# Performance work log

Hardware: AMD Instinct MI355X
Metric: run time of the kernel (lower is better)

The kernel has to match this reference:

```python
import jax, jax.numpy as jnp
import numpy as np

L, E, H, D, F, B, CIN, N = 12, 128, 4, 32, 512, 64, 256, 257


def setup_inputs() -> dict:
    key = jax.random.key(0)
    ks = jax.random.split(key, 10)
    s = 0.02
    rn = lambda k, shape: jax.random.normal(k, shape, jnp.float32) * s
    return {
        "feat": jax.random.normal(ks[0], (B, CIN, 32, 32), jnp.float32),
        "conv_w": rn(ks[1], (E, CIN, 3, 3)),
        "conv_b": jnp.zeros((E,), jnp.float32),
        "pos_emb": rn(ks[2], (1, N, E)),
        "cls_token": rn(ks[3], (1, 1, E)),
        "ln1_s": jnp.ones((L, E), jnp.float32),
        "ln1_b": jnp.zeros((L, E), jnp.float32),
        "qkv_w": rn(ks[4], (L, 3 * E, E)),
        "qkv_b": jnp.zeros((L, 3 * E), jnp.float32),
        "proj_w": rn(ks[5], (L, E, E)),
        "proj_b": jnp.zeros((L, E), jnp.float32),
        "ln2_s": jnp.ones((L, E), jnp.float32),
        "ln2_b": jnp.zeros((L, E), jnp.float32),
        "ffn1_w": rn(ks[6], (L, F, E)),
        "ffn1_b": jnp.zeros((L, F), jnp.float32),
        "ffn2_w": rn(ks[7], (L, E, F)),
        "ffn2_b": jnp.zeros((L, E), jnp.float32),
        "fn_s": jnp.ones((E,), jnp.float32),
        "fn_b": jnp.zeros((E,), jnp.float32),
        "fc_w": rn(ks[8], (2, E)),
        "fc_b": jnp.zeros((2,), jnp.float32),
    }


def _ln(x, s, b, eps):
    m = jnp.mean(x, -1, keepdims=True)
    v = jnp.mean((x - m) ** 2, -1, keepdims=True)
    return (x - m) * jax.lax.rsqrt(v + eps) * s + b


def reference(feat, conv_w, conv_b, pos_emb, cls_token, ln1_s, ln1_b, qkv_w,
              qkv_b, proj_w, proj_b, ln2_s, ln2_b, ffn1_w, ffn1_b, ffn2_w,
              ffn2_b, fn_s, fn_b, fc_w, fc_b):
    # patch embed: 3x3 conv stride 2 -> 16x16 = 256 tokens
    emb = jax.lax.conv_general_dilated(
        feat, conv_w, (2, 2), ((1, 1), (1, 1)),
        dimension_numbers=("NCHW", "OIHW", "NCHW")) + conv_b[None, :, None, None]
    Bsz = emb.shape[0]
    emb = emb.reshape(Bsz, E, -1).transpose(0, 2, 1)  # [B, 256, E]
    x = jnp.concatenate([jnp.broadcast_to(cls_token, (Bsz, 1, E)), emb], axis=1)
    x = x + pos_emb  # [B, N, E]
    scale = (E // H) ** -0.5

    def block(x, p):
        l1s, l1b, qw, qb, pw, pb, l2s, l2b, w1, b1, w2, b2 = p
        h = _ln(x, l1s, l1b, 1e-5)
        qkv = (h @ qw.T + qb).reshape(Bsz, N, 3, H, D).transpose(2, 0, 3, 1, 4)
        q, k, v = qkv[0], qkv[1], qkv[2]  # [B, H, N, D]
        att = jax.nn.softmax(jnp.einsum("bhnd,bhmd->bhnm", q, k) * scale, axis=-1)
        o = jnp.einsum("bhnm,bhmd->bhnd", att, v).transpose(0, 2, 1, 3).reshape(Bsz, N, E)
        x = x + (o @ pw.T + pb)
        h2 = _ln(x, l2s, l2b, 1e-5)
        x = x + (jax.nn.gelu(h2 @ w1.T + b1, approximate=False) @ w2.T + b2)
        return x, None

    x, _ = jax.lax.scan(block, x, (ln1_s, ln1_b, qkv_w, qkv_b, proj_w, proj_b,
                                   ln2_s, ln2_b, ffn1_w, ffn1_b, ffn2_w, ffn2_b))
    x = _ln(x, fn_s, fn_b, 1e-6)
    out_feat = x[:, 0, :]
    out = out_feat @ fc_w.T + fc_b
    return (out, out_feat)
```

## Files before the change

### kernel.cpp

```cpp
#include <hip/hip_runtime.h>
#include <math.h>

constexpr int NP_ = 272;
constexpr int MP_ = 64 * NP_;
constexpr int TPB_ = 17;

typedef short short8 __attribute__((ext_vector_type(8)));
typedef float f32x4 __attribute__((ext_vector_type(4)));

__device__ inline short f2bs(float f) {
    unsigned u = __builtin_bit_cast(unsigned, f);
    unsigned r = (u + 0x7fffu + ((u >> 16) & 1u)) >> 16;
    return (short)r;
}

__device__ inline f32x4 mfma16(short8 a, short8 b, f32x4 c) {
    return __builtin_amdgcn_mfma_f32_16x16x32_bf16(a, b, c, 0, 0, 0);
}

__global__ void repack_w(const float* __restrict__ in, short* __restrict__ out, int Nn, int K, int total) {
    int o = blockIdx.x * 256 + threadIdx.x;
    if (o >= total) return;
    int per = Nn * K;
    int l = o / per, r = o % per;
    int chunk = r / (Nn * 8);
    int w = r % (Nn * 8);
    int n = w >> 3, j = w & 7;
    int k = chunk * 8 + j;
    out[o] = f2bs(in[(size_t)l * per + (size_t)n * K + k]);
}

__global__ void conv_w_perm(const float* __restrict__ w, short* __restrict__ wr) {
    int o = blockIdx.x * 256 + threadIdx.x;
    if (o >= 128 * 2304) return;
    int j = o & 7;
    int col = (o >> 3) & 127;
    int c = o >> 10;
    int qd = c & 3, cscb = c >> 2;
    int cs = cscb & 7, kykx = cscb >> 3;
    int cin = cs * 32 + qd * 8 + j;
    int ky = kykx / 3, kx = kykx % 3;
    wr[o] = f2bs(w[((col * 256 + cin) * 3 + ky) * 3 + kx]);
}

__global__ __launch_bounds__(256) void feat_nhwc(const float* __restrict__ feat, short* __restrict__ fp) {
    __shared__ float tile[32][33];
    int b = blockIdx.x >> 5, y = blockIdx.x & 31;
    int t = threadIdx.x;
    for (int c0 = 0; c0 < 256; c0 += 32) {
        int ci = t >> 5, x = t & 31;
        for (int cc = ci; cc < 32; cc += 8)
            tile[cc][x] = feat[((size_t)(b * 256 + c0 + cc) * 32 + y) * 32 + x];
        __syncthreads();
        for (int i = t; i < 1024; i += 256) {
            int c = i & 31, x2 = i >> 5;
            fp[((size_t)(b * 34 + y + 1) * 34 + x2 + 1) * 256 + c0 + c] = f2bs(tile[c][x2]);
        }
        __syncthreads();
    }
}

__global__ __launch_bounds__(256) void conv_gemm(const short* __restrict__ fp, const short* __restrict__ wr,
                                                 const float* __restrict__ cb, const float* __restrict__ pos,
                                                 float* __restrict__ X) {
    __shared__ __align__(16) short Ain[3 * 34 * 256];
    int b = blockIdx.x >> 4, oy = blockIdx.x & 15;
    int tid = threadIdx.x;
    for (int idx = tid; idx < 3 * 34 * 32; idx += 256) {
        int r = idx / 1088, rem = idx - r * 1088;
        int x = rem >> 5, c = rem & 31;
        short8 v = *(const short8*)(fp + ((size_t)(b * 34 + 2 * oy + r) * 34 + x) * 256 + c * 8);
        *(short8*)(Ain + (r * 34 + x) * 256 + ((c ^ ((x >> 1) & 7)) * 8)) = v;
    }
    __syncthreads();
    int wave = tid >> 6, lane = tid & 63;
    int ng = wave, lo = lane & 15, qd = lane >> 4;
    f32x4 acc[2] = {};
#pragma unroll
    for (int ky = 0; ky < 3; ++ky)
#pragma unroll
        for (int kx = 0; kx < 3; ++kx) {
            int sx = 2 * lo + kx;
            int arow = (ky * 34 + sx) * 256;
            int sw = (sx >> 1) & 7;
            const short* wb = wr + (((size_t)((ky * 3 + kx) * 8) * 4 + qd) * 128 + ng * 32 + lo) * 8;
#pragma unroll
            for (int cs = 0; cs < 8; ++cs) {
                short8 af = *(const short8*)(Ain + arow + (((cs * 4 + qd) ^ sw) * 8));
                short8 b0 = *(const short8*)(wb + (size_t)cs * 4096);
                short8 b1 = *(const short8*)(wb + (size_t)cs * 4096 + 128);
                acc[0] = mfma16(af, b0, acc[0]);
                acc[1] = mfma16(af, b1, acc[1]);
            }
        }
#pragma unroll
    for (int t = 0; t < 2; ++t) {
        int e = ng * 32 + t * 16 + lo;
        float bias = cb[e];
#pragma unroll
        for (int r = 0; r < 4; ++r) {
            int tok = 1 + oy * 16 + qd * 4 + r;
            X[((size_t)b * NP_ + tok) * 128 + e] = acc[t][r] + bias + pos[tok * 128 + e];
        }
    }
}

__global__ __launch_bounds__(256) void cls_init(const float* __restrict__ cls, const float* __restrict__ pos,
                                                float* __restrict__ X) {
    int b = blockIdx.x, tid = threadIdx.x;
    if (tid < 128) X[(size_t)b * NP_ * 128 + tid] = cls[tid] + pos[tid];
    for (int idx = tid; idx < 15 * 128; idx += 256)
        X[((size_t)b * NP_ + 257) * 128 + idx] = 0.f;
}

__device__ inline void ln_frags32(const float* Xl, const float* __restrict__ s, const float* __restrict__ bb,
                                  short* aF, int tid, float eps) {
    int wv = tid >> 6, lane = tid & 63;
    int r4 = lane & 3, c32 = lane >> 2;
    int row = wv * 4 + r4;
    const float* xr = Xl + row * 132 + c32 * 8;
    float4 a = *(const float4*)(xr);
    float4 b = *(const float4*)(xr + 4);
    float v[8] = {a.x, a.y, a.z, a.w, b.x, b.y, b.z, b.w};
    float sum = v[0] + v[1] + v[2] + v[3] + v[4] + v[5] + v[6] + v[7];
    sum += __shfl_xor(sum, 4); sum += __shfl_xor(sum, 8);
    sum += __shfl_xor(sum, 16); sum += __shfl_xor(sum, 32);
    float mean = sum * (1.f / 128.f);
    float vs = 0.f;
#pragma unroll
    for (int j = 0; j < 8; ++j) { float d = v[j] - mean; vs += d * d; }
    vs += __shfl_xor(vs, 4); vs += __shfl_xor(vs, 8);
    vs += __shfl_xor(vs, 16); vs += __shfl_xor(vs, 32);
    float rs = rsqrtf(vs * (1.f / 128.f) + eps);
    float4 s0 = *(const float4*)(s + c32 * 8), s1 = *(const float4*)(s + c32 * 8 + 4);
    float4 b0 = *(const float4*)(bb + c32 * 8), b1 = *(const float4*)(bb + c32 * 8 + 4);
    float sv[8] = {s0.x, s0.y, s0.z, s0.w, s1.x, s1.y, s1.z, s1.w};
    float bv[8] = {b0.x, b0.y, b0.z, b0.w, b1.x, b1.y, b1.z, b1.w};
    short8 o;
#pragma unroll
    for (int j = 0; j < 8; ++j) o[j] = f2bs((v[j] - mean) * rs * sv[j] + bv[j]);
    *(short8*)(aF + (((row >> 4) * 16 + c32) * 16 + (row & 15)) * 8) = o;
}

__device__ inline void qkv_stage(const short* aF, const short* __restrict__ wq, const float* __restrict__ qb,
                                 int mg, int wv, int lo, int qd,
                                 short* __restrict__ Qf, short* __restrict__ Kf, short* __restrict__ Vf) {
    int n0 = wv * 48;
    f32x4 acc[2][3] = {};
#pragma unroll
    for (int ki = 0; ki < 4; ++ki) {
        int kq = ki * 4 + qd;
        short8 bf[3];
#pragma unroll
        for (int t = 0; t < 3; ++t)
            bf[t] = *(const short8*)(wq + ((size_t)kq * 384 + n0 + t * 16 + lo) * 8);
#pragma unroll
        for (int mt = 0; mt < 2; ++mt) {
            short8 a = *(const short8*)(aF + ((mt * 16 + kq) * 16 + lo) * 8);
#pragma unroll
            for (int t = 0; t < 3; ++t) acc[mt][t] = mfma16(a, bf[t], acc[mt][t]);
        }
    }
#pragma unroll
    for (int mt = 0; mt < 2; ++mt)
#pragma unroll
        for (int t = 0; t < 3; ++t) {
            int n = n0 + t * 16 + lo;
            float bvv = qb[n];
            int seg = n >> 7, m = n & 127, h = m >> 5, d = m & 31;
            short* dst = (seg == 0) ? Qf : ((seg == 1) ? Kf : Vf);
#pragma unroll
            for (int r = 0; r < 4; ++r) {
                int row = mg * 32 + mt * 16 + qd * 4 + r;
                int bb2 = row / NP_, q = row - bb2 * NP_;
                dst[((size_t)(bb2 * 4 + h) * 4 + (d >> 3)) * (NP_ * 8) + q * 8 + (d & 7)] =
                    f2bs(acc[mt][t][r] + bvv);
            }
        }
}

__global__ __launch_bounds__(512, 4) void qkv0(const float* __restrict__ X, const short* __restrict__ wq,
                                               const float* __restrict__ qb, const float* __restrict__ ls,
                                               const float* __restrict__ lb,
                                               short* __restrict__ Qf, short* __restrict__ Kf,
                                               short* __restrict__ Vf) {
    __shared__ __align__(16) float Xl[32 * 132];
    __shared__ __align__(16) short aF[2 * 16 * 16 * 8];
    int mg = blockIdx.x, tid = threadIdx.x;
    for (int idx = tid; idx < 1024; idx += 512) {
        int tok = idx >> 5, c = idx & 31;
        *(float4*)(Xl + tok * 132 + c * 4) = *(const float4*)(X + (size_t)(mg * 32 + tok) * 128 + c * 4);
    }
    __syncthreads();
    ln_frags32(Xl, ls, lb, aF, tid, 1e-5f);
    __syncthreads();
    int wv = tid >> 6, lane = tid & 63;
    qkv_stage(aF, wq, qb, mg, wv, lane & 15, lane >> 4, Qf, Kf, Vf);
}

__global__ __launch_bounds__(256, 4) void tail_a(const short* __restrict__ Of, const short* __restrict__ wp,
                                                 const float* __restrict__ pb, const float* __restrict__ l2s,
                                                 const float* __restrict__ l2b, float* __restrict__ X,
                                                 short* __restrict__ Hf) {
    __shared__ __align__(16) short AL[2 * 2048];
    __shared__ __align__(16) float Xl[32 * 132];
    int mg = blockIdx.x, tid = threadIdx.x;
    const short* osrc = Of + (size_t)mg * 4096;
    for (int idx = tid; idx < 512; idx += 256)
        *(short8*)(AL + idx * 8) = *(const short8*)(osrc + idx * 8);
    for (int idx = tid; idx < 1024; idx += 256) {
        int tok = idx >> 5, c = idx & 31;
        *(float4*)(Xl + tok * 132 + c * 4) = *(const float4*)(X + (size_t)(mg * 32 + tok) * 128 + c * 4);
    }
    __syncthreads();
    int wv = tid >> 6, lane = tid & 63, lo = lane & 15, qd = lane >> 4;
    int n0 = wv * 32;
    f32x4 acc[2][2] = {};
#pragma unroll
    for (int ki = 0; ki < 4; ++ki) {
        int kq = ki * 4 + qd;
        short8 b0 = *(const short8*)(wp + ((size_t)kq * 128 + n0 + lo) * 8);
        short8 b1 = *(const short8*)(wp + ((size_t)kq * 128 + n0 + 16 + lo) * 8);
#pragma unroll
        for (int mt = 0; mt < 2; ++mt) {
            short8 a = *(const short8*)(AL + mt * 2048 + (kq * 16 + lo) * 8);
            acc[mt][0] = mfma16(a, b0, acc[mt][0]);
            acc[mt][1] = mfma16(a, b1, acc[mt][1]);
        }
    }
    float pb0 = pb[n0 + lo], pb1 = pb[n0 + 16 + lo];
#pragma unroll
    for (int mt = 0; mt < 2; ++mt)
#pragma unroll
        for (int r = 0; r < 4; ++r) {
            int row = mt * 16 + qd * 4 + r;
            Xl[row * 132 + n0 + lo] += acc[mt][0][r] + pb0;
            Xl[row * 132 + n0 + 16 + lo] += acc[mt][1][r] + pb1;
        }
    __syncthreads();
    for (int idx = tid; idx < 1024; idx += 256) {
        int tok = idx >> 5, c = idx & 31;
        *(float4*)(X + (size_t)(mg * 32 + tok) * 128 + c * 4) = *(const float4*)(Xl + tok * 132 + c * 4);
    }
    {
        int r8 = lane & 7, c16 = lane >> 3;
        int row = wv * 8 + r8;
        const float* xr = Xl + row * 132 + c16 * 16;
        float v[16]; float sum = 0.f;
#pragma unroll
        for (int p2 = 0; p2 < 4; ++p2) {
            float4 a = *(const float4*)(xr + p2 * 4);
            v[p2 * 4 + 0] = a.x; v[p2 * 4 + 1] = a.y; v[p2 * 4 + 2] = a.z; v[p2 * 4 + 3] = a.w;
            sum += a.x + a.y + a.z + a.w;
        }
        sum += __shfl_xor(sum, 8); sum += __shfl_xor(sum, 16); sum += __shfl_xor(sum, 32);
        float mean = sum * (1.f / 128.f);
        float vs = 0.f;
#pragma unroll
        for (int j = 0; j < 16; ++j) { float d = v[j] - mean; vs += d * d; }
        vs += __shfl_xor(vs, 8); vs += __shfl_xor(vs, 16); vs += __shfl_xor(vs, 32);
        float rs = rsqrtf(vs * (1.f / 128.f) + 1e-5f);
        float sv[16], bv[16];
#pragma unroll
        for (int p2 = 0; p2 < 4; ++p2) {
            float4 a = *(const float4*)(l2s + c16 * 16 + p2 * 4);
            float4 c = *(const float4*)(l2b + c16 * 16 + p2 * 4);
            sv[p2 * 4 + 0] = a.x; sv[p2 * 4 + 1] = a.y; sv[p2 * 4 + 2] = a.z; sv[p2 * 4 + 3] = a.w;
            bv[p2 * 4 + 0] = c.x; bv[p2 * 4 + 1] = c.y; bv[p2 * 4 + 2] = c.z; bv[p2 * 4 + 3] = c.w;
        }
        short8 o0, o1;
#pragma unroll
        for (int j = 0; j < 8; ++j) {
            o0[j] = f2bs((v[j] - mean) * rs * sv[j] + bv[j]);
            o1[j] = f2bs((v[j + 8] - mean) * rs * sv[j + 8] + bv[j + 8]);
        }
        int t2 = row >> 4, mr = row & 15;
        *(short8*)(Hf + (size_t)(2 * mg + t2) * 2048 + (c16 * 2) * 128 + mr * 8) = o0;
        *(short8*)(Hf + (size_t)(2 * mg + t2) * 2048 + (c16 * 2 + 1) * 128 + mr * 8) = o1;
    }
}

template <int LAST>
__global__ __launch_bounds__(512, 4) void tail_b(const short* __restrict__ Hf, const short* __restrict__ w1,
                                                 const float* __restrict__ b1, const short* __restrict__ w2,
                                                 const float* __restrict__ b2, float* __restrict__ X,
                                                 const float* __restrict__ l1s, const float* __restrict__ l1b,
                                                 const short* __restrict__ wq, const float* __restrict__ qb,
                                                 short* __restrict__ Qf, short* __restrict__ Kf,
                                                 short* __restrict__ Vf) {
    __shared__ __align__(16) short HfL[2 * 2048];
    __shared__ __align__(16) short U[128 * 136];
    __shared__ __align__(16) float Xl[32 * 132];
    __shared__ __align__(16) short aF[2 * 16 * 16 * 8];
    int mg = blockIdx.x, tid = threadIdx.x;
    const short* hsrc = Hf + (size_t)mg * 4096;
    for (int idx = tid; idx < 512; idx += 512)
        *(short8*)(HfL + idx * 8) = *(const short8*)(hsrc + idx * 8);
    for (int idx = tid; idx < 1024; idx += 512) {
        int tok = idx >> 5, c = idx & 31;
        *(float4*)(Xl + tok * 132 + c * 4) = *(const float4*)(X + (size_t)(mg * 32 + tok) * 128 + c * 4);
    }
    __syncthreads();
    int wv = tid >> 6, lane = tid & 63, lo = lane & 15, qd = lane >> 4;
    {
        int n0 = wv * 64;
        f32x4 fa[2][4] = {};
#pragma unroll
        for (int ki = 0; ki < 4; ++ki) {
            int kq = ki * 4 + qd;
            short8 bf[4];
#pragma unroll
            for (int t = 0; t < 4; ++t)
                bf[t] = *(const short8*)(w1 + ((size_t)kq * 512 + n0 + t * 16 + lo) * 8);
#pragma unroll
            for (int mt = 0; mt < 2; ++mt) {
                short8 a = *(const short8*)(HfL + mt * 2048 + (kq * 16 + lo) * 8);
#pragma unroll
                for (int t = 0; t < 4; ++t) fa[mt][t] = mfma16(a, bf[t], fa[mt][t]);
            }
        }
#pragma unroll
        for (int t = 0; t < 4; ++t) {
            int n = n0 + t * 16 + lo;
            float bvv = b1[n];
#pragma unroll
            for (int mt = 0; mt < 2; ++mt)
#pragma unroll
                for (int r = 0; r < 4; ++r) {
                    float x = fa[mt][t][r] + bvv;
                    float u = x * (0.7978845608f + 0.0356774081f * x * x);
                    x = x / (1.f + __expf(-2.f * u));
                    U[(mt * 64 + (n >> 3)) * 136 + (qd * 4 + r) * 8 + (n & 7)] = f2bs(x);
                }
        }
    }
    __syncthreads();
    {
        int n0 = wv * 16;
        f32x4 fa[2] = {};
#pragma unroll 4
        for (int ki = 0; ki < 16; ++ki) {
            int kq = ki * 4 + qd;
            short8 bf = *(const short8*)(w2 + ((size_t)kq * 128 + n0 + lo) * 8);
#pragma unroll
            for (int mt = 0; mt < 2; ++mt) {
                short8 a = *(const short8*)(U + (mt * 64 + kq) * 136 + lo * 8);
                fa[mt] = mfma16(a, bf, fa[mt]);
            }
        }
        float bvv = b2[n0 + lo];
#pragma unroll
        for (int mt = 0; mt < 2; ++mt)
#pragma unroll
            for (int r = 0; r < 4; ++r)
                Xl[(mt * 16 + qd * 4 + r) * 132 + n0 + lo] += fa[mt][r] + bvv;
    }
    __syncthreads();
    for (int idx = tid; idx < 1024; idx += 512) {
        int tok = idx >> 5, c = idx & 31;
        *(float4*)(X + (size_t)(mg * 32 + tok) * 128 + c * 4) = *(const float4*)(Xl + tok * 132 + c * 4);
    }
    if (LAST) return;
    ln_frags32(Xl, l1s, l1b, aF, tid, 1e-5f);
    __syncthreads();
    qkv_stage(aF, wq, qb, mg, wv, lo, qd, Qf, Kf, Vf);
}

__global__ __launch_bounds__(256) void attn(const short* __restrict__ Qf, const short* __restrict__ Kf,
                                            const short* __restrict__ Vf, short* __restrict__ Of) {
    __shared__ __align__(16) short Kl[4 * NP_ * 8];
    __shared__ __align__(16) short Vl[32 * 288];
    __shared__ __align__(16) short Pl[4 * 36 * 16 * 8];
    int b = blockIdx.x >> 3, h = (blockIdx.x >> 1) & 3, half = blockIdx.x & 1;
    int tid = threadIdx.x;
    const short* kf = Kf + (size_t)(b * 4 + h) * (4 * NP_ * 8);
    const short* vf = Vf + (size_t)(b * 4 + h) * (4 * NP_ * 8);
    const short* qf = Qf + (size_t)(b * 4 + h) * (4 * NP_ * 8);
    for (int idx = tid; idx < 1088; idx += 256)
        *(short8*)(Kl + idx * 8) = *(const short8*)(kf + idx * 8);
#pragma unroll
    for (int kq = 0; kq < 4; ++kq)
        for (int q = tid; q < NP_; q += 256) {
            short8 v = *(const short8*)(vf + ((size_t)kq * NP_ + q) * 8);
#pragma unroll
            for (int j = 0; j < 8; ++j) Vl[(kq * 8 + j) * 288 + q] = v[j];
        }
    for (int idx = tid; idx < 512; idx += 256) {
        int d = idx >> 4, c = idx & 15;
        Vl[d * 288 + 272 + c] = 0;
    }
    for (int idx = tid; idx < 128; idx += 256) {
        int w = idx >> 5, t = idx & 31;
        short8 z = {};
        *(short8*)(Pl + w * 4608 + 34 * 128 + t * 8) = z;
    }
    __syncthreads();
    int wv = tid >> 6, lane = tid & 63, lo = lane & 15, qd = lane >> 4;
    short* Pw = Pl + wv * 4608;
    const float scale = 0.17677669529663687f;
    for (int it = 0; it < 3; ++it) {
        int qt = it * 8 + half * 4 + wv;
        if (qt > 16) break;
        short8 qfr = *(const short8*)(qf + ((size_t)qd * NP_ + qt * 16 + lo) * 8);
        f32x4 sc[17];
#pragma unroll
        for (int kt = 0; kt < 17; ++kt) {
            short8 kfr = *(const short8*)(Kl + ((size_t)qd * NP_ + kt * 16 + lo) * 8);
            f32x4 z = {};
            sc[kt] = mfma16(qfr, kfr, z);
        }
        float mx[4] = {-1e30f, -1e30f, -1e30f, -1e30f};
#pragma unroll
        for (int kt = 0; kt < 17; ++kt) {
            bool valid = (kt * 16 + lo) < 257;
#pragma unroll
            for (int r = 0; r < 4; ++r) {
                float v2 = valid ? sc[kt][r] * scale : -1e30f;
                sc[kt][r] = v2;
                mx[r] = fmaxf(mx[r], v2);
            }
        }
#pragma unroll
        for (int r = 0; r < 4; ++r) {
            mx[r] = fmaxf(mx[r], __shfl_xor(mx[r], 1));
            mx[r] = fmaxf(mx[r], __shfl_xor(mx[r], 2));
            mx[r] = fmaxf(mx[r], __shfl_xor(mx[r], 4));
            mx[r] = fmaxf(mx[r], __shfl_xor(mx[r], 8));
        }
        float l[4] = {0.f, 0.f, 0.f, 0.f};
#pragma unroll
        for (int kt = 0; kt < 17; ++kt)
#pragma unroll
            for (int r = 0; r < 4; ++r) {
                float p = __expf(sc[kt][r] - mx[r]);
                sc[kt][r] = p;
                l[r] += p;
            }
#pragma unroll
        for (int r = 0; r < 4; ++r) {
            l[r] += __shfl_xor(l[r], 1);
            l[r] += __shfl_xor(l[r], 2);
            l[r] += __shfl_xor(l[r], 4);
            l[r] += __shfl_xor(l[r], 8);
        }
        float rl[4];
#pragma unroll
        for (int r = 0; r < 4; ++r) rl[r] = 1.f / l[r];
#pragma unroll
        for (int kt = 0; kt < 17; ++kt)
#pragma unroll
            for (int r = 0; r < 4; ++r) {
                int key = kt * 16 + lo;
                Pw[((key >> 3) * 16 + qd * 4 + r) * 8 + (key & 7)] = f2bs(sc[kt][r] * rl[r]);
            }
        f32x4 oa[2] = {};
#pragma unroll
        for (int ks = 0; ks < 9; ++ks) {
            short8 pf = *(const short8*)(Pw + ((ks * 4 + qd) * 16 + lo) * 8);
#pragma unroll
            for (int nt = 0; nt < 2; ++nt) {
                short8 vfr = *(const short8*)(Vl + (nt * 16 + lo) * 288 + ks * 32 + qd * 8);
                oa[nt] = mfma16(pf, vfr, oa[nt]);
            }
        }
        int tile = b * TPB_ + qt;
#pragma unroll
        for (int nt = 0; nt < 2; ++nt)
#pragma unroll
            for (int r = 0; r < 4; ++r) {
                int qq = qt * 16 + qd * 4 + r;
                if (qq <= 256) {
                    int col = h * 32 + nt * 16 + lo;
                    Of[(size_t)tile * 2048 + (col >> 3) * 128 + (qd * 4 + r) * 8 + (col & 7)] = f2bs(oa[nt][r]);
                }
            }
    }
}

__global__ __launch_bounds__(64) void final_head(const float* __restrict__ X, const float* __restrict__ fs,
                                                 const float* __restrict__ fb, const float* __restrict__ fcw,
                                                 const float* __restrict__ fcb, float* __restrict__ out) {
    int b = blockIdx.x, lane = threadIdx.x;
    float2 v = *(const float2*)(X + (size_t)b * NP_ * 128 + lane * 2);
    float sum = v.x + v.y;
#pragma unroll
    for (int m = 1; m < 64; m <<= 1) sum += __shfl_xor(sum, m);
    float mean = sum * (1.f / 128.f);
    float d0 = v.x - mean, d1 = v.y - mean;
    float vs = d0 * d0 + d1 * d1;
#pragma unroll
    for (int m = 1; m < 64; m <<= 1) vs += __shfl_xor(vs, m);
    float rs = rsqrtf(vs * (1.f / 128.f) + 1e-6f);
    int e = lane * 2;
    float f0 = d0 * rs * fs[e] + fb[e];
    float f1 = d1 * rs * fs[e + 1] + fb[e + 1];
    out[128 + b * 128 + e] = f0;
    out[128 + b * 128 + e + 1] = f1;
    float p0 = f0 * fcw[e] + f1 * fcw[e + 1];
    float p1 = f0 * fcw[128 + e] + f1 * fcw[128 + e + 1];
#pragma unroll
    for (int m = 1; m < 64; m <<= 1) {
        p0 += __shfl_xor(p0, m);
        p1 += __shfl_xor(p1, m);
    }
    if (lane == 0) {
        out[b * 2 + 0] = p0 + fcb[0];
        out[b * 2 + 1] = p1 + fcb[1];
    }
}

extern "C" void kernel_launch(void* const* d_in, const int* in_sizes, int n_in,
                              void* d_out, int out_size, void* d_ws, size_t ws_size,
                              hipStream_t stream) {
    const float* feat    = (const float*)d_in[0];
    const float* conv_w  = (const float*)d_in[1];
    const float* conv_b  = (const float*)d_in[2];
    const float* pos_emb = (const float*)d_in[3];
    const float* cls_tok = (const float*)d_in[4];
    const float* ln1_s   = (const float*)d_in[5];
    const float* ln1_b   = (const float*)d_in[6];
    const float* qkv_w   = (const float*)d_in[7];
    const float* qkv_b   = (const float*)d_in[8];
    const float* proj_w  = (const float*)d_in[9];
    const float* proj_b  = (const float*)d_in[10];
    const float* ln2_s   = (const float*)d_in[11];
    const float* ln2_b   = (const float*)d_in[12];
    const float* ffn1_w  = (const float*)d_in[13];
    const float* ffn1_b  = (const float*)d_in[14];
    const float* ffn2_w  = (const float*)d_in[15];
    const float* ffn2_b  = (const float*)d_in[16];
    const float* fn_s    = (const float*)d_in[17];
    const float* fn_b    = (const float*)d_in[18];
    const float* fc_w    = (const float*)d_in[19];
    const float* fc_b    = (const float*)d_in[20];

    char* p = (char*)d_ws;
    auto alloc = [&](size_t bytes) { char* r = p; p += (bytes + 255) & ~(size_t)255; return r; };
    short* wq  = (short*)alloc((size_t)589824 * 2);
    short* wp  = (short*)alloc((size_t)196608 * 2);
    short* w1  = (short*)alloc((size_t)786432 * 2);
    short* w2  = (short*)alloc((size_t)786432 * 2);
    short* wc  = (short*)alloc((size_t)294912 * 2);
    short* fpd = (short*)alloc((size_t)64 * 34 * 34 * 256 * 2);
    float* X   = (float*)alloc((size_t)MP_ * 128 * 4);
    short* Qf  = (short*)alloc((size_t)64 * 16 * NP_ * 8 * 2);
    short* Kf  = (short*)alloc((size_t)64 * 16 * NP_ * 8 * 2);
    short* Vf  = (short*)alloc((size_t)64 * 16 * NP_ * 8 * 2);
    short* Of  = (short*)alloc((size_t)(MP_ / 16) * 2048 * 2);
    short* Hf  = (short*)alloc((size_t)(MP_ / 16) * 2048 * 2);

    hipMemsetAsync(fpd, 0, (size_t)64 * 34 * 34 * 256 * 2, stream);
    repack_w<<<2304, 256, 0, stream>>>(qkv_w, wq, 384, 128, 589824);
    repack_w<<<768, 256, 0, stream>>>(proj_w, wp, 128, 128, 196608);
    repack_w<<<3072, 256, 0, stream>>>(ffn1_w, w1, 512, 128, 786432);
    repack_w<<<3072, 256, 0, stream>>>(ffn2_w, w2, 128, 512, 786432);
    conv_w_perm<<<1152, 256, 0, stream>>>(conv_w, wc);
    feat_nhwc<<<64 * 32, 256, 0, stream>>>(feat, fpd);
    conv_gemm<<<1024, 256, 0, stream>>>(fpd, wc, conv_b, pos_emb, X);
    cls_init<<<64, 256, 0, stream>>>(cls_tok, pos_emb, X);

    qkv0<<<544, 512, 0, stream>>>(X, wq, qkv_b, ln1_s, ln1_b, Qf, Kf, Vf);
    for (int l = 0; l < 12; ++l) {
        attn<<<512, 256, 0, stream>>>(Qf, Kf, Vf, Of);
        tail_a<<<544, 256, 0, stream>>>(Of, wp + (size_t)l * 16384, proj_b + l * 128,
                                        ln2_s + l * 128, ln2_b + l * 128, X, Hf);
        if (l < 11)
            tail_b<0><<<544, 512, 0, stream>>>(Hf, w1 + (size_t)l * 65536, ffn1_b + l * 512,
                                               w2 + (size_t)l * 65536, ffn2_b + l * 128, X,
                                               ln1_s + (l + 1) * 128, ln1_b + (l + 1) * 128,
                                               wq + (size_t)(l + 1) * 49152, qkv_b + (l + 1) * 384,
                                               Qf, Kf, Vf);
        else
            tail_b<1><<<544, 512, 0, stream>>>(Hf, w1 + (size_t)l * 65536, ffn1_b + l * 512,
                                               w2 + (size_t)l * 65536, ffn2_b + l * 128, X,
                                               ln1_s, ln1_b, wq, qkv_b, Qf, Kf, Vf);
    }
    final_head<<<64, 64, 0, stream>>>(X, fn_s, fn_b, fc_w, fc_b, (float*)d_out);
}
```

Measured before the change: 870.4 us.

## Fuse proj/LN2/FFN/QKV into one 16-row layer kernel, transpose V layout

Measured after the change: 864.2 us. Within noise of the previous version (-0.7%).

```diff
diff --git a/kernel.cpp b/kernel.cpp
--- a/kernel.cpp
+++ b/kernel.cpp
@@ -18,29 +18,55 @@
     return __builtin_amdgcn_mfma_f32_16x16x32_bf16(a, b, c, 0, 0, 0);
 }
 
-__global__ void repack_w(const float* __restrict__ in, short* __restrict__ out, int Nn, int K, int total) {
+__global__ void repack_all(const float* __restrict__ qkvw, const float* __restrict__ projw,
+                           const float* __restrict__ f1w, const float* __restrict__ f2w,
+                           const float* __restrict__ convw,
+                           short* __restrict__ wq, short* __restrict__ wp,
+                           short* __restrict__ w1, short* __restrict__ w2,
+                           short* __restrict__ wc) {
     int o = blockIdx.x * 256 + threadIdx.x;
-    if (o >= total) return;
-    int per = Nn * K;
-    int l = o / per, r = o % per;
-    int chunk = r / (Nn * 8);
-    int w = r % (Nn * 8);
-    int n = w >> 3, j = w & 7;
-    int k = chunk * 8 + j;
-    out[o] = f2bs(in[(size_t)l * per + (size_t)n * K + k]);
-}
-
-__global__ void conv_w_perm(const float* __restrict__ w, short* __restrict__ wr) {
-    int o = blockIdx.x * 256 + threadIdx.x;
-    if (o >= 128 * 2304) return;
-    int j = o & 7;
-    int col = (o >> 3) & 127;
-    int c = o >> 10;
-    int qd = c & 3, cscb = c >> 2;
-    int cs = cscb & 7, kykx = cscb >> 3;
-    int cin = cs * 32 + qd * 8 + j;
-    int ky = kykx / 3, kx = kykx % 3;
-    wr[o] = f2bs(w[((col * 256 + cin) * 3 + ky) * 3 + kx]);
+    if (o < 589824) {
+        int l = o / 49152, r = o % 49152;
+        int chunk = r / 3072, w = r % 3072;
+        int n = w >> 3, k = chunk * 8 + (w & 7);
+        wq[o] = f2bs(qkvw[(size_t)l * 49152 + n * 128 + k]);
+        return;
+    }
+    o -= 589824;
+    if (o < 196608) {
+        int l = o / 16384, r = o % 16384;
+        int chunk = r / 1024, w = r % 1024;
+        int n = w >> 3, k = chunk * 8 + (w & 7);
+        wp[o] = f2bs(projw[(size_t)l * 16384 + n * 128 + k]);
+        return;
+    }
+    o -= 196608;
+    if (o < 786432) {
+        int l = o / 65536, r = o % 65536;
+        int chunk = r / 4096, w = r % 4096;
+        int n = w >> 3, k = chunk * 8 + (w & 7);
+        w1[o] = f2bs(f1w[(size_t)l * 65536 + n * 128 + k]);
+        return;
+    }
+    o -= 786432;
+    if (o < 786432) {
+        int l = o / 65536, r = o % 65536;
+        int chunk = r / 1024, w = r % 1024;
+        int n = w >> 3, k = chunk * 8 + (w & 7);
+        w2[o] = f2bs(f2w[(size_t)l * 65536 + n * 512 + k]);
+        return;
+    }
+    o -= 786432;
+    if (o < 294912) {
+        int j = o & 7;
+        int col = (o >> 3) & 127;
+        int c = o >> 10;
+        int qd = c & 3, cscb = c >> 2;
+        int cs = cscb & 7, kykx = cscb >> 3;
+        int cin = cs * 32 + qd * 8 + j;
+        int ky = kykx / 3, kx = kykx % 3;
+        wc[o] = f2bs(convw[((col * 256 + cin) * 3 + ky) * 3 + kx]);
+    }
 }
 
 __global__ __launch_bounds__(256) void feat_nhwc(const float* __restrict__ feat, short* __restrict__ fp) {
@@ -58,6 +84,16 @@
         }
         __syncthreads();
     }
+    short* rowp = fp + (size_t)(b * 34 + y + 1) * 34 * 256;
+    for (int c = t; c < 256; c += 256) { rowp[c] = 0; rowp[33 * 256 + c] = 0; }
+    if (y == 0) {
+        short* r0 = fp + (size_t)(b * 34) * 34 * 256;
+        for (int i = t; i < 34 * 256; i += 256) r0[i] = 0;
+    }
+    if (y == 31) {
+        short* r33 = fp + (size_t)(b * 34 + 33) * 34 * 256;
+        for (int i = t; i < 34 * 256; i += 256) r33[i] = 0;
+    }
 }
 
 __global__ __launch_bounds__(256) void conv_gemm(const short* __restrict__ fp, const short* __restrict__ wr,
@@ -113,8 +149,8 @@
         X[((size_t)b * NP_ + 257) * 128 + idx] = 0.f;
 }
 
-__device__ inline void ln_frags32(const float* Xl, const float* __restrict__ s, const float* __restrict__ bb,
-                                  short* aF, int tid, float eps) {
+__device__ inline void ln_tile16(const float* Xl, const float* __restrict__ s, const float* __restrict__ bb,
+                                 short* SB, int tid, float eps) {
     int wv = tid >> 6, lane = tid & 63;
     int r4 = lane & 3, c32 = lane >> 2;
     int row = wv * 4 + r4;
@@ -139,264 +175,188 @@
     short8 o;
 #pragma unroll
     for (int j = 0; j < 8; ++j) o[j] = f2bs((v[j] - mean) * rs * sv[j] + bv[j]);
-    *(short8*)(aF + (((row >> 4) * 16 + c32) * 16 + (row & 15)) * 8) = o;
-}
-
-__device__ inline void qkv_stage(const short* aF, const short* __restrict__ wq, const float* __restrict__ qb,
-                                 int mg, int wv, int lo, int qd,
-                                 short* __restrict__ Qf, short* __restrict__ Kf, short* __restrict__ Vf) {
-    int n0 = wv * 48;
-    f32x4 acc[2][3] = {};
+    *(short8*)(SB + (c32 * 16 + row) * 8) = o;
+}
+
+__device__ inline void qkv_stage16(const short* SB, const short* __restrict__ wq, const float* __restrict__ qb,
+                                   int mg, int wv, int lo, int qd,
+                                   short* __restrict__ Qf, short* __restrict__ Kf, short* __restrict__ Vt) {
+    int n0 = wv * 96;
+    f32x4 acc[6] = {};
 #pragma unroll
     for (int ki = 0; ki < 4; ++ki) {
         int kq = ki * 4 + qd;
-        short8 bf[3];
-#pragma unroll
-        for (int t = 0; t < 3; ++t)
-            bf[t] = *(const short8*)(wq + ((size_t)kq * 384 + n0 + t * 16 + lo) * 8);
-#pragma unroll
-        for (int mt = 0; mt < 2; ++mt) {
-            short8 a = *(const short8*)(aF + ((mt * 16 + kq) * 16 + lo) * 8);
-#pragma unroll
-            for (int t = 0; t < 3; ++t) acc[mt][t] = mfma16(a, bf[t], acc[mt][t]);
-        }
-    }
-#pragma unroll
-    for (int mt = 0; mt < 2; ++mt)
-#pragma unroll
-        for (int t = 0; t < 3; ++t) {
-            int n = n0 + t * 16 + lo;
-            float bvv = qb[n];
-            int seg = n >> 7, m = n & 127, h = m >> 5, d = m & 31;
-            short* dst = (seg == 0) ? Qf : ((seg == 1) ? Kf : Vf);
-#pragma unroll
-            for (int r = 0; r < 4; ++r) {
-                int row = mg * 32 + mt * 16 + qd * 4 + r;
-                int bb2 = row / NP_, q = row - bb2 * NP_;
-                dst[((size_t)(bb2 * 4 + h) * 4 + (d >> 3)) * (NP_ * 8) + q * 8 + (d & 7)] =
-                    f2bs(acc[mt][t][r] + bvv);
-            }
-        }
-}
-
-__global__ __launch_bounds__(512, 4) void qkv0(const float* __restrict__ X, const short* __restrict__ wq,
+        short8 a = *(const short8*)(SB + (kq * 16 + lo) * 8);
+#pragma unroll
+        for (int t = 0; t < 6; ++t) {
+            short8 bf = *(const short8*)(wq + ((size_t)kq * 384 + n0 + t * 16 + lo) * 8);
+            acc[t] = mfma16(a, bf, acc[t]);
+        }
+    }
+#pragma unroll
+    for (int t = 0; t < 6; ++t) {
+        int n = n0 + t * 16 + lo;
+        float bvv = qb[n];
+        int seg = n >> 7, m = n & 127, h = m >> 5, d = m & 31;
+#pragma unroll
+        for (int r = 0; r < 4; ++r) {
+            int row = mg * 16 + qd * 4 + r;
+            int bb2 = row / NP_, q = row - bb2 * NP_;
+            short val = f2bs(acc[t][r] + bvv);
+            if (seg == 2)
+                Vt[((size_t)(bb2 * 4 + h) * 32 + d) * NP_ + q] = val;
+            else
+                (seg ? Kf : Qf)[((size_t)(bb2 * 4 + h) * 4 + (d >> 3)) * (NP_ * 8) + q * 8 + (d & 7)] = val;
+        }
+    }
+}
+
+__global__ __launch_bounds__(256, 4) void qkv0(const float* __restrict__ X, const short* __restrict__ wq,
                                                const float* __restrict__ qb, const float* __restrict__ ls,
                                                const float* __restrict__ lb,
                                                short* __restrict__ Qf, short* __restrict__ Kf,
-                                               short* __restrict__ Vf) {
-    __shared__ __align__(16) float Xl[32 * 132];
-    __shared__ __align__(16) short aF[2 * 16 * 16 * 8];
+                                               short* __restrict__ Vt) {
+    __shared__ __align__(16) float Xl[16 * 132];
+    __shared__ __align__(16) short SB[2048];
     int mg = blockIdx.x, tid = threadIdx.x;
-    for (int idx = tid; idx < 1024; idx += 512) {
+    for (int idx = tid; idx < 512; idx += 256) {
         int tok = idx >> 5, c = idx & 31;
-        *(float4*)(Xl + tok * 132 + c * 4) = *(const float4*)(X + (size_t)(mg * 32 + tok) * 128 + c * 4);
-    }
-    __syncthreads();
-    ln_frags32(Xl, ls, lb, aF, tid, 1e-5f);
+        *(float4*)(Xl + tok * 132 + c * 4) = *(const float4*)(X + (size_t)(mg * 16 + tok) * 128 + c * 4);
+    }
+    __syncthreads();
+    ln_tile16(Xl, ls, lb, SB, tid, 1e-5f);
     __syncthreads();
     int wv = tid >> 6, lane = tid & 63;
-    qkv_stage(aF, wq, qb, mg, wv, lane & 15, lane >> 4, Qf, Kf, Vf);
-}
-
-__global__ __launch_bounds__(256, 4) void tail_a(const short* __restrict__ Of, const short* __restrict__ wp,
-                                                 const float* __restrict__ pb, const float* __restrict__ l2s,
-                                                 const float* __restrict__ l2b, float* __restrict__ X,
-                                                 short* __restrict__ Hf) {
-    __shared__ __align__(16) short AL[2 * 2048];
-    __shared__ __align__(16) float Xl[32 * 132];
+    qkv_stage16(SB, wq, qb, mg, wv, lane & 15, lane >> 4, Qf, Kf, Vt);
+}
+
+template <int LAST>
+__global__ __launch_bounds__(256, 4) void layer_tail(
+    const short* __restrict__ Of, const short* __restrict__ wp, const float* __restrict__ pb,
+    const float* __restrict__ l2s, const float* __restrict__ l2b,
+    const short* __restrict__ w1, const float* __restrict__ b1,
+    const short* __restrict__ w2, const float* __restrict__ b2,
+    float* __restrict__ X,
+    const float* __restrict__ l1s, const float* __restrict__ l1b,
+    const short* __restrict__ wq, const float* __restrict__ qb,
+    short* __restrict__ Qf, short* __restrict__ Kf, short* __restrict__ Vt) {
+    __shared__ __align__(16) short SB[2048];
+    __shared__ __align__(16) float Xl[16 * 132];
+    __shared__ __align__(16) short Uh[32 * 136];
     int mg = blockIdx.x, tid = threadIdx.x;
-    const short* osrc = Of + (size_t)mg * 4096;
-    for (int idx = tid; idx < 512; idx += 256)
-        *(short8*)(AL + idx * 8) = *(const short8*)(osrc + idx * 8);
-    for (int idx = tid; idx < 1024; idx += 256) {
+    const short* osrc = Of + (size_t)mg * 2048;
+    for (int idx = tid; idx < 256; idx += 256)
+        *(short8*)(SB + idx * 8) = *(const short8*)(osrc + idx * 8);
+    for (int idx = tid; idx < 512; idx += 256) {
         int tok = idx >> 5, c = idx & 31;
-        *(float4*)(Xl + tok * 132 + c * 4) = *(const float4*)(X + (size_t)(mg * 32 + tok) * 128 + c * 4);
-    }
-    __syncthreads();
-    int wv = tid >> 6, lane = tid & 63, lo = lane & 15, qd = lane >> 4;
-    int n0 = wv * 32;
-    f32x4 acc[2][2] = {};
-#pragma unroll
-    for (int ki = 0; ki < 4; ++ki) {
-        int kq = ki * 4 + qd;
-        short8 b0 = *(const short8*)(wp + ((size_t)kq * 128 + n0 + lo) * 8);
-        short8 b1 = *(const short8*)(wp + ((size_t)kq * 128 + n0 + 16 + lo) * 8);
-#pragma unroll
-        for (int mt = 0; mt < 2; ++mt) {
-            short8 a = *(const short8*)(AL + mt * 2048 + (kq * 16 + lo) * 8);
-            acc[mt][0] = mfma16(a, b0, acc[mt][0]);
-            acc[mt][1] = mfma16(a, b1, acc[mt][1]);
-        }
-    }
-    float pb0 = pb[n0 + lo], pb1 = pb[n0 + 16 + lo];
-#pragma unroll
-    for (int mt = 0; mt < 2; ++mt)
-#pragma unroll
-        for (int r = 0; r < 4; ++r) {
-            int row = mt * 16 + qd * 4 + r;
-            Xl[row * 132 + n0 + lo] += acc[mt][0][r] + pb0;
-            Xl[row * 132 + n0 + 16 + lo] += acc[mt][1][r] + pb1;
-        }
-    __syncthreads();
-    for (int idx = tid; idx < 1024; idx += 256) {
-        int tok = idx >> 5, c = idx & 31;
-        *(float4*)(X + (size_t)(mg * 32 + tok) * 128 + c * 4) = *(const float4*)(Xl + tok * 132 + c * 4);
-    }
-    {
-        int r8 = lane & 7, c16 = lane >> 3;
-        int row = wv * 8 + r8;
-        const float* xr = Xl + row * 132 + c16 * 16;
-        float v[16]; float sum = 0.f;
-#pragma unroll
-        for (int p2 = 0; p2 < 4; ++p2) {
-            float4 a = *(const float4*)(xr + p2 * 4);
-            v[p2 * 4 + 0] = a.x; v[p2 * 4 + 1] = a.y; v[p2 * 4 + 2] = a.z; v[p2 * 4 + 3] = a.w;
-            sum += a.x + a.y + a.z + a.w;
-        }
-        sum += __shfl_xor(sum, 8); sum += __shfl_xor(sum, 16); sum += __shfl_xor(sum, 32);
-        float mean = sum * (1.f / 128.f);
-        float vs = 0.f;
-#pragma unroll
-        for (int j = 0; j < 16; ++j) { float d = v[j] - mean; vs += d * d; }
-        vs += __shfl_xor(vs, 8); vs += __shfl_xor(vs, 16); vs += __shfl_xor(vs, 32);
-        float rs = rsqrtf(vs * (1.f / 128.f) + 1e-5f);
-        float sv[16], bv[16];
-#pragma unroll
-        for (int p2 = 0; p2 < 4; ++p2) {
-            float4 a = *(const float4*)(l2s + c16 * 16 + p2 * 4);
-            float4 c = *(const float4*)(l2b + c16 * 16 + p2 * 4);
-            sv[p2 * 4 + 0] = a.x; sv[p2 * 4 + 1] = a.y; sv[p2 * 4 + 2] = a.z; sv[p2 * 4 + 3] = a.w;
-            bv[p2 * 4 + 0] = c.x; bv[p2 * 4 + 1] = c.y; bv[p2 * 4 + 2] = c.z; bv[p2 * 4 + 3] = c.w;
-        }
-        short8 o0, o1;
-#pragma unroll
-        for (int j = 0; j < 8; ++j) {
-            o0[j] = f2bs((v[j] - mean) * rs * sv[j] + bv[j]);
-            o1[j] = f2bs((v[j + 8] - mean) * rs * sv[j + 8] + bv[j + 8]);
-        }
-        int t2 = row >> 4, mr = row & 15;
-        *(short8*)(Hf + (size_t)(2 * mg + t2) * 2048 + (c16 * 2) * 128 + mr * 8) = o0;
-        *(short8*)(Hf + (size_t)(2 * mg + t2) * 2048 + (c16 * 2 + 1) * 128 + mr * 8) = o1;
-    }
-}
-
-template <int LAST>
-__global__ __launch_bounds__(512, 4) void tail_b(const short* __restrict__ Hf, const short* __restrict__ w1,
-                                                 const float* __restrict__ b1, const short* __restrict__ w2,
-                                                 const float* __restrict__ b2, float* __restrict__ X,
-                                                 const float* __restrict__ l1s, const float* __restrict__ l1b,
-                                                 const short* __restrict__ wq, const float* __restrict__ qb,
-                                                 short* __restrict__ Qf, short* __restrict__ Kf,
-                                                 short* __restrict__ Vf) {
-    __shared__ __align__(16) short HfL[2 * 2048];
-    __shared__ __align__(16) short U[128 * 136];
-    __shared__ __align__(16) float Xl[32 * 132];
-    __shared__ __align__(16) short aF[2 * 16 * 16 * 8];
-    int mg = blockIdx.x, tid = threadIdx.x;
-    const short* hsrc = Hf + (size_t)mg * 4096;
-    for (int idx = tid; idx < 512; idx += 512)
-        *(short8*)(HfL + idx * 8) = *(const short8*)(hsrc + idx * 8);
-    for (int idx = tid; idx < 1024; idx += 512) {
-        int tok = idx >> 5, c = idx & 31;
-        *(float4*)(Xl + tok * 132 + c * 4) = *(const float4*)(X + (size_t)(mg * 32 + tok) * 128 + c * 4);
+        *(float4*)(Xl + tok * 132 + c * 4) = *(const float4*)(X + (size_t)(mg * 16 + tok) * 128 + c * 4);
     }
     __syncthreads();
     int wv = tid >> 6, lane = tid & 63, lo = lane & 15, qd = lane >> 4;
     {
-        int n0 = wv * 64;
-        f32x4 fa[2][4] = {};
+        int n0 = wv * 32;
+        f32x4 pa[2] = {};
 #pragma unroll
         for (int ki = 0; ki < 4; ++ki) {
             int kq = ki * 4 + qd;
-            short8 bf[4];
-#pragma unroll
-            for (int t = 0; t < 4; ++t)
-                bf[t] = *(const short8*)(w1 + ((size_t)kq * 512 + n0 + t * 16 + lo) * 8);
-#pragma unroll
-            for (int mt = 0; mt < 2; ++mt) {
-                short8 a = *(const short8*)(HfL + mt * 2048 + (kq * 16 + lo) * 8);
-#pragma unroll
-                for (int t = 0; t < 4; ++t) fa[mt][t] = mfma16(a, bf[t], fa[mt][t]);
-            }
-        }
-#pragma unroll
-        for (int t = 0; t < 4; ++t) {
-            int n = n0 + t * 16 + lo;
-            float bvv = b1[n];
-#pragma unroll
-            for (int mt = 0; mt < 2; ++mt)
+            short8 a = *(const short8*)(SB + (kq * 16 + lo) * 8);
+            short8 b0 = *(const short8*)(wp + ((size_t)kq * 128 + n0 + lo) * 8);
+            short8 b1 = *(const short8*)(wp + ((size_t)kq * 128 + n0 + 16 + lo) * 8);
+            pa[0] = mfma16(a, b0, pa[0]);
+            pa[1] = mfma16(a, b1, pa[1]);
+        }
+        float pb0 = pb[n0 + lo], pb1 = pb[n0 + 16 + lo];
+#pragma unroll
+        for (int r = 0; r < 4; ++r) {
+            Xl[(qd * 4 + r) * 132 + n0 + lo] += pa[0][r] + pb0;
+            Xl[(qd * 4 + r) * 132 + n0 + 16 + lo] += pa[1][r] + pb1;
+        }
+    }
+    __syncthreads();
+    ln_tile16(Xl, l2s, l2b, SB, tid, 1e-5f);
+    __syncthreads();
+    f32x4 facc[2] = {};
+#pragma unroll
+    for (int hh = 0; hh < 2; ++hh) {
+        {
+            int n0h = wv * 64;
+            f32x4 fa[4] = {};
+#pragma unroll
+            for (int ki = 0; ki < 4; ++ki) {
+                int kq = ki * 4 + qd;
+                short8 a = *(const short8*)(SB + (kq * 16 + lo) * 8);
+#pragma unroll
+                for (int t = 0; t < 4; ++t) {
+                    short8 bf = *(const short8*)(w1 + ((size_t)kq * 512 + hh * 256 + n0h + t * 16 + lo) * 8);
+                    fa[t] = mfma16(a, bf, fa[t]);
+                }
+            }
+#pragma unroll
+            for (int t = 0; t < 4; ++t) {
+                int nl = n0h + t * 16 + lo;
+                float bvv = b1[hh * 256 + nl];
 #pragma unroll
                 for (int r = 0; r < 4; ++r) {
-                    float x = fa[mt][t][r] + bvv;
+                    float x = fa[t][r] + bvv;
                     float u = x * (0.7978845608f + 0.0356774081f * x * x);
                     x = x / (1.f + __expf(-2.f * u));
-                    U[(mt * 64 + (n >> 3)) * 136 + (qd * 4 + r) * 8 + (n & 7)] = f2bs(x);
+                    Uh[(nl >> 3) * 136 + (qd * 4 + r) * 8 + (nl & 7)] = f2bs(x);
                 }
-        }
-    }
-    __syncthreads();
+            }
+        }
+        __syncthreads();
+        {
+            int n0 = wv * 32;
+#pragma unroll
+            for (int ki = 0; ki < 8; ++ki) {
+                int kq2 = ki * 4 + qd;
+                short8 a = *(const short8*)(Uh + kq2 * 136 + lo * 8);
+                short8 b0 = *(const short8*)(w2 + (((size_t)(hh * 32 + kq2)) * 128 + n0 + lo) * 8);
+                short8 b1 = *(const short8*)(w2 + (((size_t)(hh * 32 + kq2)) * 128 + n0 + 16 + lo) * 8);
+                facc[0] = mfma16(a, b0, facc[0]);
+                facc[1] = mfma16(a, b1, facc[1]);
+            }
+        }
+        if (hh == 0) __syncthreads();
+    }
     {
-        int n0 = wv * 16;
-        f32x4 fa[2] = {};
-#pragma unroll 4
-        for (int ki = 0; ki < 16; ++ki) {
-            int kq = ki * 4 + qd;
-            short8 bf = *(const short8*)(w2 + ((size_t)kq * 128 + n0 + lo) * 8);
-#pragma unroll
-            for (int mt = 0; mt < 2; ++mt) {
-                short8 a = *(const short8*)(U + (mt * 64 + kq) * 136 + lo * 8);
-                fa[mt] = mfma16(a, bf, fa[mt]);
-            }
-        }
-        float bvv = b2[n0 + lo];
-#pragma unroll
-        for (int mt = 0; mt < 2; ++mt)
-#pragma unroll
-            for (int r = 0; r < 4; ++r)
-                Xl[(mt * 16 + qd * 4 + r) * 132 + n0 + lo] += fa[mt][r] + bvv;
-    }
-    __syncthreads();
-    for (int idx = tid; idx < 1024; idx += 512) {
+        int n0 = wv * 32;
+        float b20 = b2[n0 + lo], b21 = b2[n0 + 16 + lo];
+#pragma unroll
+        for (int r = 0; r < 4; ++r) {
+            Xl[(qd * 4 + r) * 132 + n0 + lo] += facc[0][r] + b20;
+            Xl[(qd * 4 + r) * 132 + n0 + 16 + lo] += facc[1][r] + b21;
+        }
+    }
+    __syncthreads();
+    for (int idx = tid; idx < 512; idx += 256) {
         int tok = idx >> 5, c = idx & 31;
-        *(float4*)(X + (size_t)(mg * 32 + tok) * 128 + c * 4) = *(const float4*)(Xl + tok * 132 + c * 4);
+        *(float4*)(X + (size_t)(mg * 16 + tok) * 128 + c * 4) = *(const float4*)(Xl + tok * 132 + c * 4);
     }
     if (LAST) return;
-    ln_frags32(Xl, l1s, l1b, aF, tid, 1e-5f);
-    __syncthreads();
-    qkv_stage(aF, wq, qb, mg, wv, lo, qd, Qf, Kf, Vf);
-}
-
-__global__ __launch_bounds__(256) void attn(const short* __restrict__ Qf, const short* __restrict__ Kf,
-                                            const short* __restrict__ Vf, short* __restrict__ Of) {
-    __shared__ __align__(16) short Kl[4 * NP_ * 8];
-    __shared__ __align__(16) short Vl[32 * 288];
-    __shared__ __align__(16) short Pl[4 * 36 * 16 * 8];
+    ln_tile16(Xl, l1s, l1b, SB, tid, 1e-5f);
+    __syncthreads();
+    qkv_stage16(SB, wq, qb, mg, wv, lo, qd, Qf, Kf, Vt);
+}
+
+__global__ __launch_bounds__(256, 4) void attn(const short* __restrict__ Qf, const short* __restrict__ Kf,
+                                               const short* __restrict__ Vt, short* __restrict__ Of) {
+    __shared__ __align__(16) short Vl[32 * 296];
+    __shared__ __align__(16) short Pl[4][544];
     int b = blockIdx.x >> 3, h = (blockIdx.x >> 1) & 3, half = blockIdx.x & 1;
     int tid = threadIdx.x;
     const short* kf = Kf + (size_t)(b * 4 + h) * (4 * NP_ * 8);
-    const short* vf = Vf + (size_t)(b * 4 + h) * (4 * NP_ * 8);
     const short* qf = Qf + (size_t)(b * 4 + h) * (4 * NP_ * 8);
-    for (int idx = tid; idx < 1088; idx += 256)
-        *(short8*)(Kl + idx * 8) = *(const short8*)(kf + idx * 8);
-#pragma unroll
-    for (int kq = 0; kq < 4; ++kq)
-        for (int q = tid; q < NP_; q += 256) {
-            short8 v = *(const short8*)(vf + ((size_t)kq * NP_ + q) * 8);
-#pragma unroll
-            for (int j = 0; j < 8; ++j) Vl[(kq * 8 + j) * 288 + q] = v[j];
-        }
-    for (int idx = tid; idx < 512; idx += 256) {
-        int d = idx >> 4, c = idx & 15;
-        Vl[d * 288 + 272 + c] = 0;
-    }
-    for (int idx = tid; idx < 128; idx += 256) {
-        int w = idx >> 5, t = idx & 31;
-        short8 z = {};
-        *(short8*)(Pl + w * 4608 + 34 * 128 + t * 8) = z;
+    const short* vt = Vt + (size_t)(b * 4 + h) * (32 * NP_);
+    for (int idx = tid; idx < 32 * 37; idx += 256) {
+        int d = idx / 37, c8 = idx - d * 37;
+        short8 v = {};
+        if (c8 < 34) v = *(const short8*)(vt + d * NP_ + c8 * 8);
+        *(short8*)(Vl + d * 296 + c8 * 8) = v;
     }
     __syncthreads();
     int wv = tid >> 6, lane = tid & 63, lo = lane & 15, qd = lane >> 4;
-    short* Pw = Pl + wv * 4608;
+    short* Pw = Pl[wv];
     const float scale = 0.17677669529663687f;
     for (int it = 0; it < 3; ++it) {
         int qt = it * 8 + half * 4 + wv;
@@ -405,7 +365,7 @@
         f32x4 sc[17];
 #pragma unroll
         for (int kt = 0; kt < 17; ++kt) {
-            short8 kfr = *(const short8*)(Kl + ((size_t)qd * NP_ + kt * 16 + lo) * 8);
+            short8 kfr = *(const short8*)(kf + ((size_t)qd * NP_ + kt * 16 + lo) * 8);
             f32x4 z = {};
             sc[kt] = mfma16(qfr, kfr, z);
         }
@@ -446,20 +406,23 @@
         float rl[4];
 #pragma unroll
         for (int r = 0; r < 4; ++r) rl[r] = 1.f / l[r];
-#pragma unroll
-        for (int kt = 0; kt < 17; ++kt)
-#pragma unroll
-            for (int r = 0; r < 4; ++r) {
-                int key = kt * 16 + lo;
-                Pw[((key >> 3) * 16 + qd * 4 + r) * 8 + (key & 7)] = f2bs(sc[kt][r] * rl[r]);
-            }
         f32x4 oa[2] = {};
 #pragma unroll
         for (int ks = 0; ks < 9; ++ks) {
-            short8 pf = *(const short8*)(Pw + ((ks * 4 + qd) * 16 + lo) * 8);
+#pragma unroll
+            for (int kt2 = 0; kt2 < 2; ++kt2) {
+                int kt = ks * 2 + kt2;
+                int lkey = kt2 * 16 + lo;
+#pragma unroll
+                for (int r = 0; r < 4; ++r) {
+                    short pv = (kt < 17) ? f2bs(sc[kt][r] * rl[r]) : (short)0;
+                    Pw[(lkey >> 3) * 128 + (qd * 4 + r) * 8 + (lkey & 7)] = pv;
+                }
+            }
+            short8 pf = *(const short8*)(Pw + (qd * 16 + lo) * 8);
 #pragma unroll
             for (int nt = 0; nt < 2; ++nt) {
-                short8 vfr = *(const short8*)(Vl + (nt * 16 + lo) * 288 + ks * 32 + qd * 8);
+                short8 vfr = *(const short8*)(Vl + (nt * 16 + lo) * 296 + ks * 32 + qd * 8);
                 oa[nt] = mfma16(pf, vfr, oa[nt]);
             }
         }
@@ -545,35 +508,31 @@
     float* X   = (float*)alloc((size_t)MP_ * 128 * 4);
     short* Qf  = (short*)alloc((size_t)64 * 16 * NP_ * 8 * 2);
     short* Kf  = (short*)alloc((size_t)64 * 16 * NP_ * 8 * 2);
-    short* Vf  = (short*)alloc((size_t)64 * 16 * NP_ * 8 * 2);
+    short* Vt  = (short*)alloc((size_t)64 * 4 * 32 * NP_ * 2);
     short* Of  = (short*)alloc((size_t)(MP_ / 16) * 2048 * 2);
-    short* Hf  = (short*)alloc((size_t)(MP_ / 16) * 2048 * 2);
-
-    hipMemsetAsync(fpd, 0, (size_t)64 * 34 * 34 * 256 * 2, stream);
-    repack_w<<<2304, 256, 0, stream>>>(qkv_w, wq, 384, 128, 589824);
-    repack_w<<<768, 256, 0, stream>>>(proj_w, wp, 128, 128, 196608);
-    repack_w<<<3072, 256, 0, stream>>>(ffn1_w, w1, 512, 128, 786432);
-    repack_w<<<3072, 256, 0, stream>>>(ffn2_w, w2, 128, 512, 786432);
-    conv_w_perm<<<1152, 256, 0, stream>>>(conv_w, wc);
+
+    repack_all<<<10368, 256, 0, stream>>>(qkv_w, proj_w, ffn1_w, ffn2_w, conv_w, wq, wp, w1, w2, wc);
     feat_nhwc<<<64 * 32, 256, 0, stream>>>(feat, fpd);
     conv_gemm<<<1024, 256, 0, stream>>>(fpd, wc, conv_b, pos_emb, X);
     cls_init<<<64, 256, 0, stream>>>(cls_tok, pos_emb, X);
 
-    qkv0<<<544, 512, 0, stream>>>(X, wq, qkv_b, ln1_s, ln1_b, Qf, Kf, Vf);
+    qkv0<<<1088, 256, 0, stream>>>(X, wq, qkv_b, ln1_s, ln1_b, Qf, Kf, Vt);
     for (int l = 0; l < 12; ++l) {
-        attn<<<512, 256, 0, stream>>>(Qf, Kf, Vf, Of);
-        tail_a<<<544, 256, 0, stream>>>(Of, wp + (size_t)l * 16384, proj_b + l * 128,
-                                        ln2_s + l * 128, ln2_b + l * 128, X, Hf);
+        attn<<<512, 256, 0, stream>>>(Qf, Kf, Vt, Of);
         if (l < 11)
-            tail_b<0><<<544, 512, 0, stream>>>(Hf, w1 + (size_t)l * 65536, ffn1_b + l * 512,
-                                               w2 + (size_t)l * 65536, ffn2_b + l * 128, X,
-                                               ln1_s + (l + 1) * 128, ln1_b + (l + 1) * 128,
-                                               wq + (size_t)(l + 1) * 49152, qkv_b + (l + 1) * 384,
-                                               Qf, Kf, Vf);
+            layer_tail<0><<<1088, 256, 0, stream>>>(Of, wp + (size_t)l * 16384, proj_b + l * 128,
+                                                    ln2_s + l * 128, ln2_b + l * 128,
+                                                    w1 + (size_t)l * 65536, ffn1_b + l * 512,
+                                                    w2 + (size_t)l * 65536, ffn2_b + l * 128, X,
+                                                    ln1_s + (l + 1) * 128, ln1_b + (l + 1) * 128,
+                                                    wq + (size_t)(l + 1) * 49152, qkv_b + (l + 1) * 384,
+                                                    Qf, Kf, Vt);
         else
-            tail_b<1><<<544, 512, 0, stream>>>(Hf, w1 + (size_t)l * 65536, ffn1_b + l * 512,
-                                               w2 + (size_t)l * 65536, ffn2_b + l * 128, X,
-                                               ln1_s, ln1_b, wq, qkv_b, Qf, Kf, Vf);
+            layer_tail<1><<<1088, 256, 0, stream>>>(Of, wp + (size_t)l * 16384, proj_b + l * 128,
+                                                    ln2_s + l * 128, ln2_b + l * 128,
+                                                    w1 + (size_t)l * 65536, ffn1_b + l * 512,
+                                                    w2 + (size_t)l * 65536, ffn2_b + l * 128, X,
+                                                    ln1_s, ln1_b, wq, qkv_b, Qf, Kf, Vt);
     }
     final_head<<<64, 64, 0, stream>>>(X, fn_s, fn_b, fc_w, fc_b, (float*)d_out);
 }
```
